# Performance work log

Measured on AMD Instinct MI355X. Metric: run time of the kernel, lower is better.

The kernel has to match this reference:

```python
import jax, jax.numpy as jnp
import numpy as np

BANDWIDTH = 1.0
EPS = 1e-20


def setup_inputs() -> dict:
    key = jax.random.key(0)
    k1, k2, k3 = jax.random.split(key, 3)
    test_X = jax.random.normal(k1, (8192, 64), dtype=jnp.float32)
    train_X = jax.random.normal(k2, (16384, 64), dtype=jnp.float32)
    sample_weight = jax.random.uniform(k3, (16384,), dtype=jnp.float32)
    return {"test_X": test_X, "train_X": train_X, "sample_weight": sample_weight}


def reference(test_X, train_X, sample_weight):
    # test_X: [m, d], train_X: [n, d], sample_weight: [n]
    d = train_X.shape[1]
    h = jnp.float32(BANDWIDTH)
    # weights are normalized; with weights, n is treated as 1 => log(n) = 0
    w = sample_weight / jnp.sum(sample_weight)
    Z = 0.5 * d * jnp.log(2.0 * jnp.float32(np.pi)) + d * jnp.log(h)
    # squared L2 distances via expansion (avoids [m, n, d] intermediate)
    t2 = jnp.sum(test_X * test_X, axis=-1)  # [m]
    r2 = jnp.sum(train_X * train_X, axis=-1)  # [n]
    cross = test_X @ train_X.T  # [m, n]
    sq = (t2[:, None] + r2[None, :] - 2.0 * cross) / (h * h)  # [m, n]
    val = -0.5 * sq - Z  # [m, n]
    # weighted, numerically-stable log-sum-exp over train dim
    m_max = jnp.max(val, axis=-1, keepdims=True)  # [m, 1]
    s = jnp.sum(jnp.exp(val - m_max) * w[None, :], axis=-1)  # [m]
    return m_max[:, 0] + jnp.log(s + EPS)
```

## Files before the change

### kernel.cpp

```cpp
#include <hip/hip_runtime.h>
#include <hip/hip_bf16.h>
#include <math.h>

#define M 8192
#define N 16384
#define D 64
#define ZC 58.81206612509905f
#define B0 24.0f
#define LOG2E 1.4426950408889634f
#define HL2E 0.7213475204444817f
#define LN2 0.6931471805599453f

#define PCH 16
#define NCHK (N / PCH)

typedef short v8bf __attribute__((ext_vector_type(8)));
typedef float v16f __attribute__((ext_vector_type(16)));

#define B_AU2  0
#define B_PART 32768

__global__ __launch_bounds__(256, 4) void gk_main(const float* __restrict__ testX,
                                                  const float* __restrict__ trainX,
                                                  const float* __restrict__ sw,
                                                  float* __restrict__ au2,
                                                  float* __restrict__ part) {
    __shared__ __align__(16) char smem[33280];
    const int tid = threadIdx.x;
    const int w = tid >> 6;
    const int lane = tid & 63;
    const int c = lane & 31;
    const int h = lane >> 5;
    const int rl = lane >> 3;
    const int kb = lane & 7;

    const int bid = blockIdx.x;
    const int xcd = bid & 7;
    const int j = bid >> 3;
    const int chunk = xcd * 2 + (j & 1);
    const int m0 = (j >> 1) * 128;
    const int n0 = chunk * NCHK;

#pragma unroll
    for (int i = 0; i < 4; ++i) {
        int rr = w * 32 + i * 8 + rl;
        const float4* p = reinterpret_cast<const float4*>(testX + (size_t)(m0 + rr) * D + kb * 8);
        float4 v0 = p[0], v1 = p[1];
        float t2 = v0.x * v0.x + v0.y * v0.y + v0.z * v0.z + v0.w * v0.w
                 + v1.x * v1.x + v1.y * v1.y + v1.z * v1.z + v1.w * v1.w;
        t2 += __shfl_xor(t2, 1, 64);
        t2 += __shfl_xor(t2, 2, 64);
        t2 += __shfl_xor(t2, 4, 64);
        if (chunk == 0 && kb == 0) au2[m0 + rr] = -HL2E * t2;
        union { __hip_bfloat16 hx[8]; uint4 u; } cv;
        cv.hx[0] = __float2bfloat16(v0.x * LOG2E);
        cv.hx[1] = __float2bfloat16(v0.y * LOG2E);
        cv.hx[2] = __float2bfloat16(v0.z * LOG2E);
        cv.hx[3] = __float2bfloat16(v0.w * LOG2E);
        cv.hx[4] = __float2bfloat16(v1.x * LOG2E);
        cv.hx[5] = __float2bfloat16(v1.y * LOG2E);
        cv.hx[6] = __float2bfloat16(v1.z * LOG2E);
        cv.hx[7] = __float2bfloat16(v1.w * LOG2E);
        *reinterpret_cast<uint4*>(smem + kb * 2048 + ((rr ^ kb) * 16)) = cv.u;
    }
    __syncthreads();

    v8bf af[4];
#pragma unroll
    for (int t = 0; t < 4; ++t) {
        int kk = 2 * t + h;
        af[t] = *reinterpret_cast<const v8bf*>(smem + kk * 2048 + (((w * 32 + c) ^ kk) * 16));
    }

    float srun[16];
#pragma unroll
    for (int r = 0; r < 16; ++r) srun[r] = 0.f;

    char* Bs = smem + 16384;
    float* Lw = reinterpret_cast<float*>(smem + 32768);

    for (int tile = 0; tile < NCHK / 128; ++tile) {
        __syncthreads();
        const int nt0 = n0 + tile * 128;
#pragma unroll
        for (int i = 0; i < 4; ++i) {
            int rr = w * 32 + i * 8 + rl;
            float swv = sw[nt0 + rr];
            const float4* p = reinterpret_cast<const float4*>(trainX + (size_t)(nt0 + rr) * D + kb * 8);
            float4 v0 = p[0], v1 = p[1];
            float r2 = v0.x * v0.x + v0.y * v0.y + v0.z * v0.z + v0.w * v0.w
                     + v1.x * v1.x + v1.y * v1.y + v1.z * v1.z + v1.w * v1.w;
            r2 += __shfl_xor(r2, 1, 64);
            r2 += __shfl_xor(r2, 2, 64);
            r2 += __shfl_xor(r2, 4, 64);
            if (kb == 0) Lw[rr] = __builtin_amdgcn_logf(swv) - HL2E * r2 + B0;
            union { __hip_bfloat16 hx[8]; uint4 u; } cv;
            cv.hx[0] = __float2bfloat16(v0.x);
            cv.hx[1] = __float2bfloat16(v0.y);
            cv.hx[2] = __float2bfloat16(v0.z);
            cv.hx[3] = __float2bfloat16(v0.w);
            cv.hx[4] = __float2bfloat16(v1.x);
            cv.hx[5] = __float2bfloat16(v1.y);
            cv.hx[6] = __float2bfloat16(v1.z);
            cv.hx[7] = __float2bfloat16(v1.w);
            *reinterpret_cast<uint4*>(Bs + kb * 2048 + ((rr ^ kb) * 16)) = cv.u;
        }
        __syncthreads();

#pragma unroll
        for (int s = 0; s < 4; ++s) {
            float lwv = Lw[s * 32 + c];
            v16f acc;
#pragma unroll
            for (int r = 0; r < 16; ++r) acc[r] = lwv;
#pragma unroll
            for (int t = 0; t < 4; ++t) {
                int kk = 2 * t + h;
                v8bf bf = *reinterpret_cast<const v8bf*>(Bs + kk * 2048 + (((s * 32 + c) ^ kk) * 16));
                acc = __builtin_amdgcn_mfma_f32_32x32x16_bf16(af[t], bf, acc, 0, 0, 0);
            }
#pragma unroll
            for (int r = 0; r < 16; ++r)
                srun[r] += __builtin_amdgcn_exp2f(acc[r]);
        }
    }

    __syncthreads();
    float* red = reinterpret_cast<float*>(smem);
#pragma unroll
    for (int r = 0; r < 16; ++r) {
        int rowl = (r & 3) + 8 * (r >> 2) + 4 * h;
        red[(w * 32 + rowl) * 33 + c] = srun[r];
    }
    __syncthreads();
    if (tid < 128) {
        float G = 0.f;
#pragma unroll
        for (int c2 = 0; c2 < 32; ++c2) G += red[tid * 33 + c2];
        part[(size_t)chunk * M + m0 + tid] = G;
    }
}

__global__ __launch_bounds__(256) void gk_merge(const float* __restrict__ part,
                                                const float* __restrict__ au2,
                                                const float* __restrict__ sw,
                                                float* __restrict__ out) {
    __shared__ float red[256];
    const int tid = threadIdx.x;
    float s = 0.f;
    const float4* p4 = reinterpret_cast<const float4*>(sw);
    for (int i = tid; i < N / 4; i += 256) {
        float4 v = p4[i];
        s += v.x + v.y + v.z + v.w;
    }
    red[tid] = s;
    __syncthreads();
    for (int off = 128; off > 0; off >>= 1) {
        if (tid < off) red[tid] += red[tid + off];
        __syncthreads();
    }
    const float W = red[0];

    const int r = blockIdx.x * 256 + tid;
    float G = 0.f;
#pragma unroll
    for (int p = 0; p < PCH; ++p) G += part[(size_t)p * M + r];
    out[r] = LN2 * (au2[r] + __builtin_amdgcn_logf(fmaxf(G, 1e-30f)) - B0
                   - __builtin_amdgcn_logf(W)) - ZC;
}

extern "C" void kernel_launch(void* const* d_in, const int* in_sizes, int n_in,
                              void* d_out, int out_size, void* d_ws, size_t ws_size,
                              hipStream_t stream) {
    const float* testX  = (const float*)d_in[0];
    const float* trainX = (const float*)d_in[1];
    const float* sw     = (const float*)d_in[2];
    float* out = (float*)d_out;
    char* wsb = (char*)d_ws;

    float* au2  = (float*)(wsb + B_AU2);
    float* part = (float*)(wsb + B_PART);

    gk_main<<<(M / 128) * PCH, 256, 0, stream>>>(testX, trainX, sw, au2, part);
    gk_merge<<<M / 256, 256, 0, stream>>>(part, au2, sw, out);
}
```

Before: 105.5 us.

## Precompute bf16 operands and train-row bias in a separate prep kernel

Adds a prep kernel that converts test and train rows to bf16 once, computes the test norms, and precomputes the per-train-row log-weight-minus-norm bias into workspace. The main kernel then loads pre-converted bf16 tiles and the precomputed bias instead of redoing fp32 loads, norms and conversions for every tile in every block. Shared memory per block drops and the occupancy hint rises from 4 to 6 blocks. The split factor doubles to 32 chunks, which doubles the partial-sum traffic in the merge kernel and adds one extra kernel launch.

Measured after the change: 207.8 us. 97.0% more time.

```diff
diff --git a/kernel.cpp b/kernel.cpp
--- a/kernel.cpp
+++ b/kernel.cpp
@@ -11,21 +11,75 @@
 #define HL2E 0.7213475204444817f
 #define LN2 0.6931471805599453f
 
-#define PCH 16
+#define PCH 32
 #define NCHK (N / PCH)
 
 typedef short v8bf __attribute__((ext_vector_type(8)));
 typedef float v16f __attribute__((ext_vector_type(16)));
 
 #define B_AU2  0
-#define B_PART 32768
-
-__global__ __launch_bounds__(256, 4) void gk_main(const float* __restrict__ testX,
-                                                  const float* __restrict__ trainX,
-                                                  const float* __restrict__ sw,
-                                                  float* __restrict__ au2,
+#define B_LW2  32768
+#define B_PART 98304
+#define B_TB   1146880
+#define B_TR   2195456
+
+__global__ __launch_bounds__(256) void gk_prep(const float* __restrict__ testX,
+                                               const float* __restrict__ trainX,
+                                               const float* __restrict__ sw,
+                                               __hip_bfloat16* __restrict__ tb,
+                                               __hip_bfloat16* __restrict__ rb,
+                                               float* __restrict__ au2,
+                                               float* __restrict__ lw2) {
+    const int tid = threadIdx.x;
+    const int e = tid & 7;
+    if (blockIdx.x < M / 32) {
+        const int row = blockIdx.x * 32 + (tid >> 3);
+        const float4* p = reinterpret_cast<const float4*>(testX + (size_t)row * D + e * 8);
+        float4 v0 = p[0], v1 = p[1];
+        float t2 = v0.x * v0.x + v0.y * v0.y + v0.z * v0.z + v0.w * v0.w
+                 + v1.x * v1.x + v1.y * v1.y + v1.z * v1.z + v1.w * v1.w;
+        t2 += __shfl_xor(t2, 1, 64);
+        t2 += __shfl_xor(t2, 2, 64);
+        t2 += __shfl_xor(t2, 4, 64);
+        if (e == 0) au2[row] = -HL2E * t2;
+        union { __hip_bfloat16 h[8]; uint4 u; } cv;
+        cv.h[0] = __float2bfloat16(v0.x * LOG2E);
+        cv.h[1] = __float2bfloat16(v0.y * LOG2E);
+        cv.h[2] = __float2bfloat16(v0.z * LOG2E);
+        cv.h[3] = __float2bfloat16(v0.w * LOG2E);
+        cv.h[4] = __float2bfloat16(v1.x * LOG2E);
+        cv.h[5] = __float2bfloat16(v1.y * LOG2E);
+        cv.h[6] = __float2bfloat16(v1.z * LOG2E);
+        cv.h[7] = __float2bfloat16(v1.w * LOG2E);
+        *reinterpret_cast<uint4*>(tb + (size_t)row * D + e * 8) = cv.u;
+    } else {
+        const int row = (blockIdx.x - M / 32) * 32 + (tid >> 3);
+        const float4* p = reinterpret_cast<const float4*>(trainX + (size_t)row * D + e * 8);
+        float4 v0 = p[0], v1 = p[1];
+        float r2 = v0.x * v0.x + v0.y * v0.y + v0.z * v0.z + v0.w * v0.w
+                 + v1.x * v1.x + v1.y * v1.y + v1.z * v1.z + v1.w * v1.w;
+        r2 += __shfl_xor(r2, 1, 64);
+        r2 += __shfl_xor(r2, 2, 64);
+        r2 += __shfl_xor(r2, 4, 64);
+        if (e == 0) lw2[row] = __builtin_amdgcn_logf(sw[row]) - HL2E * r2 + B0;
+        union { __hip_bfloat16 h[8]; uint4 u; } cv;
+        cv.h[0] = __float2bfloat16(v0.x);
+        cv.h[1] = __float2bfloat16(v0.y);
+        cv.h[2] = __float2bfloat16(v0.z);
+        cv.h[3] = __float2bfloat16(v0.w);
+        cv.h[4] = __float2bfloat16(v1.x);
+        cv.h[5] = __float2bfloat16(v1.y);
+        cv.h[6] = __float2bfloat16(v1.z);
+        cv.h[7] = __float2bfloat16(v1.w);
+        *reinterpret_cast<uint4*>(rb + (size_t)row * D + e * 8) = cv.u;
+    }
+}
+
+__global__ __launch_bounds__(256, 6) void gk_main(const __hip_bfloat16* __restrict__ ta,
+                                                  const __hip_bfloat16* __restrict__ tr,
+                                                  const float* __restrict__ lw2,
                                                   float* __restrict__ part) {
-    __shared__ __align__(16) char smem[33280];
+    __shared__ __align__(16) char smem[17408];
     const int tid = threadIdx.x;
     const int w = tid >> 6;
     const int lane = tid & 63;
@@ -37,47 +91,22 @@
     const int bid = blockIdx.x;
     const int xcd = bid & 7;
     const int j = bid >> 3;
-    const int chunk = xcd * 2 + (j & 1);
-    const int m0 = (j >> 1) * 128;
+    const int chunk = xcd * 4 + (j & 3);
+    const int m0 = (j >> 2) * 128;
     const int n0 = chunk * NCHK;
 
-#pragma unroll
-    for (int i = 0; i < 4; ++i) {
-        int rr = w * 32 + i * 8 + rl;
-        const float4* p = reinterpret_cast<const float4*>(testX + (size_t)(m0 + rr) * D + kb * 8);
-        float4 v0 = p[0], v1 = p[1];
-        float t2 = v0.x * v0.x + v0.y * v0.y + v0.z * v0.z + v0.w * v0.w
-                 + v1.x * v1.x + v1.y * v1.y + v1.z * v1.z + v1.w * v1.w;
-        t2 += __shfl_xor(t2, 1, 64);
-        t2 += __shfl_xor(t2, 2, 64);
-        t2 += __shfl_xor(t2, 4, 64);
-        if (chunk == 0 && kb == 0) au2[m0 + rr] = -HL2E * t2;
-        union { __hip_bfloat16 hx[8]; uint4 u; } cv;
-        cv.hx[0] = __float2bfloat16(v0.x * LOG2E);
-        cv.hx[1] = __float2bfloat16(v0.y * LOG2E);
-        cv.hx[2] = __float2bfloat16(v0.z * LOG2E);
-        cv.hx[3] = __float2bfloat16(v0.w * LOG2E);
-        cv.hx[4] = __float2bfloat16(v1.x * LOG2E);
-        cv.hx[5] = __float2bfloat16(v1.y * LOG2E);
-        cv.hx[6] = __float2bfloat16(v1.z * LOG2E);
-        cv.hx[7] = __float2bfloat16(v1.w * LOG2E);
-        *reinterpret_cast<uint4*>(smem + kb * 2048 + ((rr ^ kb) * 16)) = cv.u;
-    }
-    __syncthreads();
-
+    const __hip_bfloat16* arow = ta + (size_t)(m0 + w * 32 + c) * D;
     v8bf af[4];
 #pragma unroll
-    for (int t = 0; t < 4; ++t) {
-        int kk = 2 * t + h;
-        af[t] = *reinterpret_cast<const v8bf*>(smem + kk * 2048 + (((w * 32 + c) ^ kk) * 16));
-    }
+    for (int t = 0; t < 4; ++t)
+        af[t] = *reinterpret_cast<const v8bf*>(arow + (2 * t + h) * 8);
 
     float srun[16];
 #pragma unroll
     for (int r = 0; r < 16; ++r) srun[r] = 0.f;
 
-    char* Bs = smem + 16384;
-    float* Lw = reinterpret_cast<float*>(smem + 32768);
+    char* Bs = smem;
+    float* Lw = reinterpret_cast<float*>(smem + 16384);
 
     for (int tile = 0; tile < NCHK / 128; ++tile) {
         __syncthreads();
@@ -85,26 +114,10 @@
 #pragma unroll
         for (int i = 0; i < 4; ++i) {
             int rr = w * 32 + i * 8 + rl;
-            float swv = sw[nt0 + rr];
-            const float4* p = reinterpret_cast<const float4*>(trainX + (size_t)(nt0 + rr) * D + kb * 8);
-            float4 v0 = p[0], v1 = p[1];
-            float r2 = v0.x * v0.x + v0.y * v0.y + v0.z * v0.z + v0.w * v0.w
-                     + v1.x * v1.x + v1.y * v1.y + v1.z * v1.z + v1.w * v1.w;
-            r2 += __shfl_xor(r2, 1, 64);
-            r2 += __shfl_xor(r2, 2, 64);
-            r2 += __shfl_xor(r2, 4, 64);
-            if (kb == 0) Lw[rr] = __builtin_amdgcn_logf(swv) - HL2E * r2 + B0;
-            union { __hip_bfloat16 hx[8]; uint4 u; } cv;
-            cv.hx[0] = __float2bfloat16(v0.x);
-            cv.hx[1] = __float2bfloat16(v0.y);
-            cv.hx[2] = __float2bfloat16(v0.z);
-            cv.hx[3] = __float2bfloat16(v0.w);
-            cv.hx[4] = __float2bfloat16(v1.x);
-            cv.hx[5] = __float2bfloat16(v1.y);
-            cv.hx[6] = __float2bfloat16(v1.z);
-            cv.hx[7] = __float2bfloat16(v1.w);
-            *reinterpret_cast<uint4*>(Bs + kb * 2048 + ((rr ^ kb) * 16)) = cv.u;
+            uint4 v = *reinterpret_cast<const uint4*>(tr + (size_t)(nt0 + rr) * D + kb * 8);
+            *reinterpret_cast<uint4*>(Bs + kb * 2048 + ((rr ^ kb) * 16)) = v;
         }
+        if (tid < 128) Lw[tid] = lw2[nt0 + tid];
         __syncthreads();
 
 #pragma unroll
@@ -179,8 +192,12 @@
     char* wsb = (char*)d_ws;
 
     float* au2  = (float*)(wsb + B_AU2);
+    float* lw2  = (float*)(wsb + B_LW2);
     float* part = (float*)(wsb + B_PART);
-
-    gk_main<<<(M / 128) * PCH, 256, 0, stream>>>(testX, trainX, sw, au2, part);
+    __hip_bfloat16* tb = (__hip_bfloat16*)(wsb + B_TB);
+    __hip_bfloat16* rb = (__hip_bfloat16*)(wsb + B_TR);
+
+    gk_prep<<<M / 32 + N / 32, 256, 0, stream>>>(testX, trainX, sw, tb, rb, au2, lw2);
+    gk_main<<<(M / 128) * PCH, 256, 0, stream>>>(tb, rb, lw2, part);
     gk_merge<<<M / 256, 256, 0, stream>>>(part, au2, sw, out);
 }
```
